# Performance work log

Hardware: AMD Instinct MI355X
Metric: run time of the kernel (lower is better)

The kernel has to match this reference:

```python
import jax, jax.numpy as jnp
import numpy as np
import math

D_MODEL = 512
H = 8
DK = D_MODEL // H  # 64
DFF = 2048
EPS = 1e-5


def layernorm(x, g, b):
    mu = jnp.mean(x, axis=-1, keepdims=True)
    var = jnp.mean((x - mu) ** 2, axis=-1, keepdims=True)
    return (x - mu) * jax.lax.rsqrt(var + EPS) * g + b


def gelu(x):
    return jax.nn.gelu(x, approximate=False)  # torch nn.GELU default (erf)


def feedforward(x, W1, b1, lng, lnb, W2, b2):
    x1 = jnp.einsum('btd,df->btf', x, W1) + b1
    x1 = gelu(layernorm(x1, lng, lnb))
    return jnp.einsum('btf,fd->btd', x1, W2) + b2


def setup_inputs() -> dict:
    key = jax.random.key(0)
    ks = iter(jax.random.split(key, 32))
    s = 0.02
    d = {}
    d['x'] = jax.random.normal(next(ks), (4, 2048, D_MODEL), jnp.float32)
    # per-head QKV projections, stacked over heads: [H, d_model, dk]
    d['Wq'] = jax.random.normal(next(ks), (H, D_MODEL, DK), jnp.float32) * s
    d['bq'] = jnp.zeros((H, DK), jnp.float32)
    d['Wk'] = jax.random.normal(next(ks), (H, D_MODEL, DK), jnp.float32) * s
    d['bk'] = jnp.zeros((H, DK), jnp.float32)
    d['Wv'] = jax.random.normal(next(ks), (H, D_MODEL, DK), jnp.float32) * s
    d['bv'] = jnp.zeros((H, DK), jnp.float32)
    d['Wo'] = jax.random.normal(next(ks), (D_MODEL, D_MODEL), jnp.float32) * s
    d['bo'] = jnp.zeros((D_MODEL,), jnp.float32)
    d['ln1_g'] = jnp.ones((D_MODEL,), jnp.float32)
    d['ln1_b'] = jnp.zeros((D_MODEL,), jnp.float32)
    # main FFN
    d['ff_W1'] = jax.random.normal(next(ks), (D_MODEL, DFF), jnp.float32) * s
    d['ff_b1'] = jnp.zeros((DFF,), jnp.float32)
    d['ff_lng'] = jnp.ones((DFF,), jnp.float32)
    d['ff_lnb'] = jnp.zeros((DFF,), jnp.float32)
    d['ff_W2'] = jax.random.normal(next(ks), (DFF, D_MODEL), jnp.float32) * s
    d['ff_b2'] = jnp.zeros((D_MODEL,), jnp.float32)
    d['ln2_g'] = jnp.ones((D_MODEL,), jnp.float32)
    d['ln2_b'] = jnp.zeros((D_MODEL,), jnp.float32)
    d['alphaA'] = jnp.zeros((1,), jnp.float32) + 0.1
    d['alphaB'] = jnp.zeros((1,), jnp.float32) + 0.1
    d['p1'] = jnp.asarray(0.1, jnp.float32)
    # sub1 FFN
    d['s1_W1'] = jax.random.normal(next(ks), (D_MODEL, DFF), jnp.float32) * s
    d['s1_b1'] = jnp.zeros((DFF,), jnp.float32)
    d['s1_lng'] = jnp.ones((DFF,), jnp.float32)
    d['s1_lnb'] = jnp.zeros((DFF,), jnp.float32)
    d['s1_W2'] = jax.random.normal(next(ks), (DFF, D_MODEL), jnp.float32) * s
    d['s1_b2'] = jnp.zeros((D_MODEL,), jnp.float32)
    d['lnsub1_g'] = jnp.ones((D_MODEL,), jnp.float32)
    d['lnsub1_b'] = jnp.zeros((D_MODEL,), jnp.float32)
    d['p2'] = jnp.asarray(0.1, jnp.float32)
    d['sub2_W'] = jax.random.normal(next(ks), (D_MODEL, D_MODEL), jnp.float32) * s
    d['sub2_b'] = jnp.zeros((D_MODEL,), jnp.float32)
    d['lnsub2_g'] = jnp.ones((D_MODEL,), jnp.float32)
    d['lnsub2_b'] = jnp.zeros((D_MODEL,), jnp.float32)
    return d


def reference(x, Wq, bq, Wk, bk, Wv, bv, Wo, bo, ln1_g, ln1_b,
              ff_W1, ff_b1, ff_lng, ff_lnb, ff_W2, ff_b2, ln2_g, ln2_b,
              alphaA, alphaB, p1, s1_W1, s1_b1, s1_lng, s1_lnb, s1_W2, s1_b2,
              lnsub1_g, lnsub1_b, p2, sub2_W, sub2_b, lnsub2_g, lnsub2_b):
    # --- multi-head attention (q = k = v = x) ---
    q = jnp.einsum('btd,hdk->bhtk', x, Wq) + bq[:, None, :]
    k = jnp.einsum('btd,hdk->bhtk', x, Wk) + bk[:, None, :]
    v = jnp.einsum('btd,hdk->bhtk', x, Wv) + bv[:, None, :]
    scores = jnp.einsum('bhtk,bhsk->bhts', q, k) / math.sqrt(DK)
    probs = jax.nn.softmax(scores, axis=-1)
    heads = jnp.einsum('bhts,bhsv->bhtv', probs, v)           # [B,H,T,dv]
    B, _, T, _ = heads.shape
    cat = jnp.transpose(heads, (0, 2, 1, 3)).reshape(B, T, H * DK)
    attn = jnp.einsum('btd,de->bte', cat, Wo) + bo
    # --- residual stack ---
    ln1 = layernorm(x + attn, ln1_g, ln1_b)
    out1 = x + ln1 * alphaA
    fft = feedforward(out1, ff_W1, ff_b1, ff_lng, ff_lnb, ff_W2, ff_b2)
    ln2 = layernorm(fft + out1, ln2_g, ln2_b)
    out2 = out1 + ln2 * alphaB
    # --- sub-branch 1 ---
    sub1 = feedforward(x, s1_W1, s1_b1, s1_lng, s1_lnb, s1_W2, s1_b2)
    sub1 = p1 * gelu(layernorm(sub1, lnsub1_g, lnsub1_b))
    # --- sub-branch 2 ---
    sub2 = jnp.einsum('btd,de->bte', x, sub2_W) + sub2_b
    sub2 = p2 * gelu(layernorm(sub2, lnsub2_g, lnsub2_b))
    return out2 + sub1 + sub2
```

## Files before the change

### kernel.cpp

```cpp
#include <hip/hip_runtime.h>
#include <hip/hip_bf16.h>
#include <math.h>

typedef __hip_bfloat16 bf16;
typedef __attribute__((ext_vector_type(8))) short s8v;
typedef __attribute__((ext_vector_type(4))) float f4v;

#define T_SEQ 2048
#define ROWS 8192
#define DMODEL 512
#define DFF 2048
#define QS 4096

#define GL2LDS(g, l) __builtin_amdgcn_global_load_lds( \
    (const __attribute__((address_space(1))) void*)(g), \
    (__attribute__((address_space(3))) void*)(l), 16, 0, 0)

__device__ __forceinline__ float b2f(bf16 v) { return __bfloat162float(v); }
__device__ __forceinline__ bf16 f2b(float v) { return __float2bfloat16(v); }
__device__ __forceinline__ float us2f(unsigned short u) {
    union { float f; unsigned int u; } c; c.u = ((unsigned int)u) << 16; return c.f;
}
__device__ __forceinline__ unsigned short f2us(float v) {
    bf16 b = f2b(v); return *(unsigned short*)&b;
}
__device__ __forceinline__ float gelu_f(float x) {
    return 0.5f * x * (1.0f + erff(x * 0.70710678118654752440f));
}
__device__ __forceinline__ float ldP(const void* p, int i, bool f32) {
    return f32 ? ((const float*)p)[i] : b2f(((const bf16*)p)[i]);
}

#define XB_E 4194304
#define RP_E 5505024
__global__ __launch_bounds__(256) void prep_all(
    const void* __restrict__ x,
    const void* Wq, const void* Wk, const void* Wv, const void* s2W,
    const void* s1W1, const void* ffW1, const void* ffW2, const void* s1W2,
    const void* Wo,
    const void* bq, const void* bk, const void* bv, const void* s2b,
    const void* s1b1, const void* bo, const void* ffb1, const void* ffb2,
    const void* s1b2,
    unsigned short* __restrict__ xb, unsigned short* __restrict__ Wbig2,
    unsigned short* __restrict__ ffW1t, unsigned short* __restrict__ ffW2t,
    unsigned short* __restrict__ s1W2t, unsigned short* __restrict__ Wot,
    float* __restrict__ bias_all, int* __restrict__ flag)
{
    __shared__ float red[4];
    __shared__ int lf;
    int tid = threadIdx.x;
    {
        float v = b2f(((const bf16*)x)[tid]);
        if (!(v == v)) v = 1e30f;
        float mx = fabsf(v);
        #pragma unroll
        for (int o = 32; o; o >>= 1) mx = fmaxf(mx, __shfl_down(mx, o));
        if ((tid & 63) == 0) red[tid >> 6] = mx;
        __syncthreads();
        if (tid == 0)
            lf = (fmaxf(fmaxf(red[0], red[1]), fmaxf(red[2], red[3])) > 1000.f) ? 1 : 0;
        __syncthreads();
    }
    bool f32 = lf != 0;
    if (blockIdx.x == 0 && tid == 0) flag[0] = lf;

    int idx = blockIdx.x * 256 + tid;
    if (idx < XB_E) {
        xb[idx] = f2us(ldP(x, idx, f32));
        return;
    }
    idx -= XB_E;
    if (idx < RP_E) {
        if (idx < 2097152) {
            int n = idx >> 9, d = idx & 511;
            float v;
            if (n < 1536) {
                int sec = n >> 9, nn = n & 511;
                int h = nn >> 6, j = nn & 63;
                const void* W = sec == 0 ? Wq : (sec == 1 ? Wk : Wv);
                v = ldP(W, (h * 512 + d) * 64 + j, f32);
            } else if (n < 2048) {
                v = ldP(s2W, d * 512 + (n - 1536), f32);
            } else {
                v = ldP(s1W1, d * 2048 + (n - 2048), f32);
            }
            Wbig2[idx] = f2us(v);
        } else if (idx < 3145728) {
            int i2 = idx - 2097152;
            int n = i2 >> 9, kd = i2 & 511;
            ffW1t[i2] = f2us(ldP(ffW1, kd * 2048 + n, f32));
        } else if (idx < 4194304) {
            int i2 = idx - 3145728;
            int n = i2 >> 11, kd = i2 & 2047;
            ffW2t[i2] = f2us(ldP(ffW2, kd * 512 + n, f32));
        } else if (idx < 5242880) {
            int i2 = idx - 4194304;
            int n = i2 >> 11, kd = i2 & 2047;
            s1W2t[i2] = f2us(ldP(s1W2, kd * 512 + n, f32));
        } else {
            int i2 = idx - 5242880;
            int n = i2 >> 9, kd = i2 & 511;
            Wot[i2] = f2us(ldP(Wo, kd * 512 + n, f32));
        }
        return;
    }
    idx -= RP_E;
    if (idx < 7680) {
        const void* src; int off;
        if      (idx < 512)  { src = bq;   off = idx; }
        else if (idx < 1024) { src = bk;   off = idx - 512; }
        else if (idx < 1536) { src = bv;   off = idx - 1024; }
        else if (idx < 2048) { src = s2b;  off = idx - 1536; }
        else if (idx < 4096) { src = s1b1; off = idx - 2048; }
        else if (idx < 4608) { src = bo;   off = idx - 4096; }
        else if (idx < 6656) { src = ffb1; off = idx - 4608; }
        else if (idx < 7168) { src = ffb2; off = idx - 6656; }
        else                 { src = s1b2; off = idx - 7168; }
        bias_all[idx] = ldP(src, off, f32);
    }
}

__device__ __forceinline__ void gemm_core(
    unsigned short* __restrict__ As, unsigned short* __restrict__ Bs,
    const unsigned short* __restrict__ A, int lda,
    const unsigned short* __restrict__ Bt,
    const float* __restrict__ bias,
    void* __restrict__ Cd, int ldc, int Kst,
    int kOff, int kLen, int doBias, int outBf16, int bm, int bn,
    unsigned short* __restrict__ Vt)
{
    int tid = threadIdx.x;
    int wave = tid >> 6, lane = tid & 63;
    int wm = wave >> 1, wn = wave & 1;
    int quad = lane >> 4, l16 = lane & 15;
    f4v acc[4][4] = {};
    int rsub = lane >> 3;
    int kcst = lane & 7;
    for (int k0 = kOff; k0 < kOff + kLen; k0 += 64) {
        #pragma unroll
        for (int i = 0; i < 4; i++) {
            int rowT = wave * 32 + i * 8 + rsub;
            int kc = (kcst - rowT) & 7;
            GL2LDS(A + (size_t)(bm + rowT) * lda + k0 + kc * 8,
                   &As[(wave * 32 + i * 8) * 64]);
            GL2LDS(Bt + (size_t)(bn + rowT) * Kst + k0 + kc * 8,
                   &Bs[(wave * 32 + i * 8) * 64]);
        }
        __syncthreads();
        #pragma unroll
        for (int ks = 0; ks < 64; ks += 32) {
            int kchunk = (ks >> 3) + quad;
            s8v af[4], bfr[4];
            #pragma unroll
            for (int mi = 0; mi < 4; mi++) {
                int m = wm * 64 + mi * 16 + l16;
                af[mi] = *(const s8v*)&As[m * 64 + (((kchunk + m) & 7) * 8)];
            }
            #pragma unroll
            for (int ni = 0; ni < 4; ni++) {
                int n = wn * 64 + ni * 16 + l16;
                bfr[ni] = *(const s8v*)&Bs[n * 64 + (((kchunk + n) & 7) * 8)];
            }
            #pragma unroll
            for (int mi = 0; mi < 4; mi++)
                #pragma unroll
                for (int ni = 0; ni < 4; ni++)
                    acc[mi][ni] = __builtin_amdgcn_mfma_f32_16x16x32_bf16(
                        af[mi], bfr[ni], acc[mi][ni], 0, 0, 0);
        }
        __syncthreads();
    }
    float bcol[4];
    #pragma unroll
    for (int ni = 0; ni < 4; ni++)
        bcol[ni] = doBias ? bias[bn + wn * 64 + ni * 16 + l16] : 0.f;
    #pragma unroll
    for (int mi = 0; mi < 4; mi++) {
        #pragma unroll
        for (int rg = 0; rg < 4; rg++) {
            size_t row = bm + wm * 64 + mi * 16 + quad * 4 + rg;
            #pragma unroll
            for (int ni = 0; ni < 4; ni++) {
                int col = bn + wn * 64 + ni * 16 + l16;
                float v = acc[mi][ni][rg] + bcol[ni];
                if (outBf16) ((unsigned short*)Cd)[row * ldc + col] = f2us(v);
                else         ((float*)Cd)[row * ldc + col] = v;
                if (Vt && col >= 1024 && col < 1536) {
                    int hd = col - 1024;
                    int b = (int)(row >> 11), t = (int)(row & 2047);
                    Vt[((size_t)b * 512 + hd) * 2048 + t] = f2us(v);
                }
            }
        }
    }
}

__global__ __launch_bounds__(256) void gemm_mfma(const unsigned short* __restrict__ A, int lda,
                                                 const unsigned short* __restrict__ Bt,
                                                 const float* __restrict__ bias,
                                                 void* __restrict__ C0,
                                                 void* __restrict__ C1,
                                                 int ldc, int K, int kLen, int outBf16,
                                                 unsigned short* __restrict__ Vt) {
    __shared__ unsigned short As[128 * 64];
    __shared__ unsigned short Bs[128 * 64];
    int z = blockIdx.z;
    gemm_core(As, Bs, A, lda, Bt, bias, z ? C1 : C0, ldc, K,
              z * kLen, kLen, z == 0, outBf16,
              blockIdx.y * 128, blockIdx.x * 128, Vt);
}

__global__ __launch_bounds__(256) void gemm_pair(
    const unsigned short* __restrict__ A1, int lda1,
    const unsigned short* __restrict__ Bt1, const float* __restrict__ bias1,
    void* __restrict__ C1a, void* __restrict__ C1b, int K1,
    const unsigned short* __restrict__ A2, int lda2,
    const unsigned short* __restrict__ Bt2, const float* __restrict__ bias2,
    void* __restrict__ C2a, void* __restrict__ C2b, int K2) {
    __shared__ unsigned short As[128 * 64];
    __shared__ unsigned short Bs[128 * 64];
    int z = blockIdx.z;
    if (z < 2) {
        int kLen = K1 / 2;
        gemm_core(As, Bs, A1, lda1, Bt1, bias1, z ? C1b : C1a, 512, K1,
                  z * kLen, kLen, z == 0, 1, blockIdx.y * 128, blockIdx.x * 128, nullptr);
    } else {
        int zz = z - 2, kLen = K2 / 2;
        gemm_core(As, Bs, A2, lda2, Bt2, bias2, zz ? C2b : C2a, 512, K2,
                  zz * kLen, kLen, zz == 0, 1, blockIdx.y * 128, blockIdx.x * 128, nullptr);
    }
}

#define ALD 72
#define SCL2 0.18033688f
__global__ __launch_bounds__(256) void attn_mfma(const unsigned short* __restrict__ QKV,
                                                 const unsigned short* __restrict__ Vt,
                                                 unsigned short* __restrict__ O) {
    __shared__ unsigned short Qs[64 * ALD];
    __shared__ unsigned short Ks[64 * ALD];
    __shared__ unsigned short Vts[64 * ALD];
    __shared__ unsigned short Ps[64 * ALD];

    int tid = threadIdx.x;
    int wave = tid >> 6, lane = tid & 63;
    int quad = lane >> 4, l16 = lane & 15;
    int qbase = blockIdx.x * 64;
    int bh = blockIdx.y;
    int b = bh >> 3, h = bh & 7;
    const unsigned short* Qg = QKV + ((size_t)(b * T_SEQ + qbase)) * QS + h * 64;
    const unsigned short* Kg = QKV + ((size_t)b * T_SEQ) * QS + 512 + h * 64;
    const unsigned short* Vtg = Vt + (size_t)bh * 64 * T_SEQ;

    int r = tid >> 3, c = (tid & 7) * 8;
    #pragma unroll
    for (int it = 0; it < 2; it++) {
        int rr = r + it * 32;
        uint4 v = *(const uint4*)(Qg + (size_t)rr * QS + c);
        *(uint4*)&Qs[rr * ALD + c] = v;
    }
    float lrun[4] = {0.f, 0.f, 0.f, 0.f};
    f4v oacc[4] = {};
    __syncthreads();

    for (int kt = 0; kt < 32; ++kt) {
        #pragma unroll
        for (int it = 0; it < 2; it++) {
            int rr = r + it * 32;
            uint4 kv = *(const uint4*)(Kg + (size_t)(kt * 64 + rr) * QS + c);
            *(uint4*)&Ks[rr * ALD + c] = kv;
            uint4 vv = *(const uint4*)(Vtg + (size_t)rr * T_SEQ + kt * 64 + c);
            *(uint4*)&Vts[rr * ALD + c] = vv;
        }
        __syncthreads();

        f4v sacc[4] = {};
        #pragma unroll
        for (int kc2 = 0; kc2 < 2; kc2++) {
            s8v aq = *(const s8v*)&Qs[(wave * 16 + l16) * ALD + kc2 * 32 + quad * 8];
            #pragma unroll
            for (int ni = 0; ni < 4; ni++) {
                s8v bk_ = *(const s8v*)&Ks[(ni * 16 + l16) * ALD + kc2 * 32 + quad * 8];
                sacc[ni] = __builtin_amdgcn_mfma_f32_16x16x32_bf16(aq, bk_, sacc[ni], 0, 0, 0);
            }
        }
        #pragma unroll
        for (int rg = 0; rg < 4; rg++) {
            #pragma unroll
            for (int ni = 0; ni < 4; ni++) {
                float p = exp2f(fminf(sacc[ni][rg] * SCL2, 30.f));
                lrun[rg] += p;
                Ps[(wave * 16 + quad * 4 + rg) * ALD + ni * 16 + l16] = f2us(p);
            }
        }
        #pragma unroll
        for (int kc2 = 0; kc2 < 2; kc2++) {
            s8v ap = *(const s8v*)&Ps[(wave * 16 + l16) * ALD + kc2 * 32 + quad * 8];
            #pragma unroll
            for (int ni = 0; ni < 4; ni++) {
                s8v bv_ = *(const s8v*)&Vts[(ni * 16 + l16) * ALD + kc2 * 32 + quad * 8];
                oacc[ni] = __builtin_amdgcn_mfma_f32_16x16x32_bf16(ap, bv_, oacc[ni], 0, 0, 0);
            }
        }
        __syncthreads();
    }

    #pragma unroll
    for (int rg = 0; rg < 4; rg++) {
        float l = lrun[rg];
        #pragma unroll
        for (int o = 8; o; o >>= 1) l += __shfl_xor(l, o);
        float linv = 1.0f / l;
        size_t orow = ((size_t)(b * T_SEQ + qbase + wave * 16 + quad * 4 + rg)) * 512 + h * 64;
        #pragma unroll
        for (int ni = 0; ni < 4; ni++)
            O[orow + ni * 16 + l16] = f2us(oacc[ni][rg] * linv);
    }
}

__global__ __launch_bounds__(256) void ln_res1(const void* __restrict__ Xraw,
                                               const unsigned short* __restrict__ Ya,
                                               const unsigned short* __restrict__ Yb,
                                               const void* __restrict__ g,
                                               const void* __restrict__ bb,
                                               const void* __restrict__ alpha,
                                               float* __restrict__ out,
                                               unsigned short* __restrict__ outb,
                                               const int* __restrict__ flag) {
    __shared__ float red[8];
    bool f32 = flag[0] != 0;
    int row = blockIdx.x, tid = threadIdx.x;
    size_t base = (size_t)row * DMODEL;
    float x0 = ldP(Xraw, base + tid, f32);
    float x1 = ldP(Xraw, base + tid + 256, f32);
    float v0 = x0 + us2f(Ya[base + tid]) + us2f(Yb[base + tid]);
    float v1 = x1 + us2f(Ya[base + tid + 256]) + us2f(Yb[base + tid + 256]);
    float s = v0 + v1, s2 = v0 * v0 + v1 * v1;
    #pragma unroll
    for (int o = 32; o; o >>= 1) { s += __shfl_down(s, o); s2 += __shfl_down(s2, o); }
    if ((tid & 63) == 0) { red[tid >> 6] = s; red[4 + (tid >> 6)] = s2; }
    __syncthreads();
    s = red[0] + red[1] + red[2] + red[3];
    s2 = red[4] + red[5] + red[6] + red[7];
    float mu = s * (1.0f / 512.0f);
    float var = s2 * (1.0f / 512.0f) - mu * mu;
    float rr = rsqrtf(var + 1e-5f);
    float a = ldP(alpha, 0, f32);
    float o0 = x0 + a * ((v0 - mu) * rr * ldP(g, tid, f32) + ldP(bb, tid, f32));
    float o1 = x1 + a * ((v1 - mu) * rr * ldP(g, tid + 256, f32) + ldP(bb, tid + 256, f32));
    out[base + tid] = o0;
    out[base + tid + 256] = o1;
    outb[base + tid] = f2us(o0);
    outb[base + tid + 256] = f2us(o1);
}

__global__ __launch_bounds__(256) void ln_gelu(unsigned short* __restrict__ Hm, int stride,
                                               const void* __restrict__ g,
                                               const void* __restrict__ bb,
                                               const int* __restrict__ flag) {
    __shared__ float red[8];
    bool f32 = flag[0] != 0;
    int row = blockIdx.x, tid = threadIdx.x;
    size_t base = (size_t)row * stride;
    float v[8];
    float s = 0.f, s2 = 0.f;
    #pragma unroll
    for (int i = 0; i < 8; i++) {
        v[i] = us2f(Hm[base + tid + i * 256]);
        s += v[i]; s2 += v[i] * v[i];
    }
    #pragma unroll
    for (int o = 32; o; o >>= 1) { s += __shfl_down(s, o); s2 += __shfl_down(s2, o); }
    if ((tid & 63) == 0) { red[tid >> 6] = s; red[4 + (tid >> 6)] = s2; }
    __syncthreads();
    s = red[0] + red[1] + red[2] + red[3];
    s2 = red[4] + red[5] + red[6] + red[7];
    float mu = s * (1.0f / 2048.0f);
    float var = s2 * (1.0f / 2048.0f) - mu * mu;
    float r = rsqrtf(var + 1e-5f);
    #pragma unroll
    for (int i = 0; i < 8; i++) {
        int cc = tid + i * 256;
        float ln = (v[i] - mu) * r * ldP(g, cc, f32) + ldP(bb, cc, f32);
        Hm[base + cc] = f2us(gelu_f(ln));
    }
}

__global__ __launch_bounds__(256) void final2(const float* __restrict__ out1,
                                              const float* __restrict__ fft,
                                              const float* __restrict__ fft2,
                                              const unsigned short* __restrict__ S1,
                                              const unsigned short* __restrict__ S1b,
                                              const unsigned short* __restrict__ S2,
                                              const void* __restrict__ g2ln,
                                              const void* __restrict__ b2ln,
                                              const void* __restrict__ alphaB,
                                              const void* __restrict__ g1s,
                                              const void* __restrict__ b1s,
                                              const void* __restrict__ g2s,
                                              const void* __restrict__ b2s,
                                              const void* __restrict__ p1,
                                              const void* __restrict__ p2,
                                              void* __restrict__ out,
                                              const int* __restrict__ flag) {
    __shared__ float red[24];
    bool f32 = flag[0] != 0;
    int row = blockIdx.x, tid = threadIdx.x;
    size_t base = (size_t)row * DMODEL;
    size_t base2 = (size_t)row * QS;
    float x0 = out1[base + tid], x1 = out1[base + tid + 256];
    float v0 = x0 + fft[base + tid] + fft2[base + tid];
    float v1 = x1 + fft[base + tid + 256] + fft2[base + tid + 256];
    float a0 = us2f(S1[base + tid]) + us2f(S1b[base + tid]);
    float a1 = us2f(S1[base + tid + 256]) + us2f(S1b[base + tid + 256]);
    float c0 = us2f(S2[base2 + tid]);
    float c1 = us2f(S2[base2 + tid + 256]);
    float sv = v0 + v1, sv2 = v0 * v0 + v1 * v1;
    float sa = a0 + a1, sa2 = a0 * a0 + a1 * a1;
    float sc = c0 + c1, sc2 = c0 * c0 + c1 * c1;
    #pragma unroll
    for (int o = 32; o; o >>= 1) {
        sv += __shfl_down(sv, o); sv2 += __shfl_down(sv2, o);
        sa += __shfl_down(sa, o); sa2 += __shfl_down(sa2, o);
        sc += __shfl_down(sc, o); sc2 += __shfl_down(sc2, o);
    }
    int w = tid >> 6;
    if ((tid & 63) == 0) {
        red[w] = sv; red[4 + w] = sv2; red[8 + w] = sa;
        red[12 + w] = sa2; red[16 + w] = sc; red[20 + w] = sc2;
    }
    __syncthreads();
    sv = red[0] + red[1] + red[2] + red[3];
    sv2 = red[4] + red[5] + red[6] + red[7];
    sa = red[8] + red[9] + red[10] + red[11];
    sa2 = red[12] + red[13] + red[14] + red[15];
    sc = red[16] + red[17] + red[18] + red[19];
    sc2 = red[20] + red[21] + red[22] + red[23];
    float muv = sv * (1.0f / 512.0f), varv = sv2 * (1.0f / 512.0f) - muv * muv;
    float rv = rsqrtf(varv + 1e-5f);
    float mua = sa * (1.0f / 512.0f), vara = sa2 * (1.0f / 512.0f) - mua * mua;
    float ra = rsqrtf(vara + 1e-5f);
    float muc = sc * (1.0f / 512.0f), varc = sc2 * (1.0f / 512.0f) - muc * muc;
    float rc = rsqrtf(varc + 1e-5f);
    float aB = ldP(alphaB, 0, f32);
    float fp1 = ldP(p1, 0, f32), fp2 = ldP(p2, 0, f32);
    float xv[2] = {x0, x1}, vv[2] = {v0, v1}, av[2] = {a0, a1}, cv[2] = {c0, c1};
    #pragma unroll
    for (int i = 0; i < 2; i++) {
        int cc = tid + i * 256;
        float out2 = xv[i] + aB * ((vv[i] - muv) * rv * ldP(g2ln, cc, f32) + ldP(b2ln, cc, f32));
        float l1 = (av[i] - mua) * ra * ldP(g1s, cc, f32) + ldP(b1s, cc, f32);
        float l2 = (cv[i] - muc) * rc * ldP(g2s, cc, f32) + ldP(b2s, cc, f32);
        float o = out2 + fp1 * gelu_f(l1) + fp2 * gelu_f(l2);
        if (f32) ((float*)out)[base + cc] = o;
        else     ((bf16*)out)[base + cc] = f2b(o);
    }
}

extern "C" void kernel_launch(void* const* d_in, const int* in_sizes, int n_in,
                              void* d_out, int out_size, void* d_ws, size_t ws_size,
                              hipStream_t stream) {
    (void)in_sizes; (void)n_in; (void)out_size; (void)ws_size;
    const void* x      = d_in[0];
    const void* Wq     = d_in[1];
    const void* bq     = d_in[2];
    const void* Wk     = d_in[3];
    const void* bk     = d_in[4];
    const void* Wv     = d_in[5];
    const void* bv     = d_in[6];
    const void* Wo     = d_in[7];
    const void* bo     = d_in[8];
    const void* ln1_g  = d_in[9];
    const void* ln1_b  = d_in[10];
    const void* ffW1   = d_in[11];
    const void* ffb1   = d_in[12];
    const void* fflng  = d_in[13];
    const void* fflnb  = d_in[14];
    const void* ffW2   = d_in[15];
    const void* ffb2   = d_in[16];
    const void* ln2_g  = d_in[17];
    const void* ln2_b  = d_in[18];
    const void* alphaA = d_in[19];
    const void* alphaB = d_in[20];
    const void* p1     = d_in[21];
    const void* s1W1   = d_in[22];
    const void* s1b1   = d_in[23];
    const void* s1lng  = d_in[24];
    const void* s1lnb  = d_in[25];
    const void* s1W2   = d_in[26];
    const void* s1b2   = d_in[27];
    const void* lns1g  = d_in[28];
    const void* lns1b  = d_in[29];
    const void* p2     = d_in[30];
    const void* s2W    = d_in[31];
    const void* s2b    = d_in[32];
    const void* lns2g  = d_in[33];
    const void* lns2b  = d_in[34];

    char* base = (char*)d_ws;
    size_t off = 0;
    auto alloc = [&](size_t bytes) {
        char* p = base + off;
        off += (bytes + 255) & ~(size_t)255;
        return p;
    };
    int* flag             = (int*)alloc(256);
    unsigned short* Wbig2 = (unsigned short*)alloc((size_t)4096 * 512 * 2);
    unsigned short* ffW1t = (unsigned short*)alloc((size_t)2048 * 512 * 2);
    unsigned short* ffW2t = (unsigned short*)alloc((size_t)512 * 2048 * 2);
    unsigned short* s1W2t = (unsigned short*)alloc((size_t)512 * 2048 * 2);
    unsigned short* Wot   = (unsigned short*)alloc(512 * 512 * 2);
    float* bias_all       = (float*)alloc(7680 * 4);
    char*  regX           = alloc((size_t)ROWS * 512 * 2);
    char*  regCat         = alloc((size_t)ROWS * 512 * 2);
    unsigned short* Cbig2 = (unsigned short*)alloc((size_t)ROWS * QS * 2);
    char*  regB           = alloc((size_t)ROWS * 512 * 2);
    char*  regD           = alloc((size_t)ROWS * 512 * 2);
    float* out1           = (float*)alloc((size_t)ROWS * 512 * 4);
    char*  regO           = alloc((size_t)ROWS * 512 * 4);

    unsigned short* xb    = (unsigned short*)regX;
    unsigned short* out1b = (unsigned short*)regX;
    unsigned short* catb  = (unsigned short*)regCat;
    float* fft            = (float*)regX;
    unsigned short* sub1raw  = (unsigned short*)regB;
    unsigned short* sub1raw2 = (unsigned short*)regD;
    unsigned short* Vtb   = (unsigned short*)regO;
    unsigned short* attnA = (unsigned short*)regO;
    unsigned short* attnB = (unsigned short*)(regO + (size_t)ROWS * 512 * 2);
    float* fft2           = (float*)regO;

    float* biasBig = bias_all + 0;
    float* biasWo  = bias_all + 4096;
    float* biasF1  = bias_all + 4608;
    float* biasF2  = bias_all + 6656;
    float* biasS12 = bias_all + 7168;

    prep_all<<<(XB_E + RP_E + 7680) / 256, 256, 0, stream>>>(
        x, Wq, Wk, Wv, s2W, s1W1, ffW1, ffW2, s1W2, Wo,
        bq, bk, bv, s2b, s1b1, bo, ffb1, ffb2, s1b2,
        xb, Wbig2, ffW1t, ffW2t, s1W2t, Wot, bias_all, flag);

    gemm_mfma<<<dim3(32, 64, 1), 256, 0, stream>>>(
        xb, 512, Wbig2, biasBig, Cbig2, nullptr, 4096, 512, 512, 1, Vtb);

    attn_mfma<<<dim3(T_SEQ / 64, 32), 256, 0, stream>>>(Cbig2, Vtb, catb);

    ln_gelu<<<ROWS, 256, 0, stream>>>(Cbig2 + 2048, QS, s1lng, s1lnb, flag);

    gemm_pair<<<dim3(4, 64, 4), 256, 0, stream>>>(
        Cbig2 + 2048, QS, s1W2t, biasS12, sub1raw, sub1raw2, 2048,
        catb, 512, Wot, biasWo, attnA, attnB, 512);

    ln_res1<<<ROWS, 256, 0, stream>>>(x, attnA, attnB, ln1_g, ln1_b, alphaA,
                                      out1, out1b, flag);

    gemm_mfma<<<dim3(16, 64, 1), 256, 0, stream>>>(
        out1b, 512, ffW1t, biasF1, Cbig2 + 2048, nullptr, 4096, 512, 512, 1, nullptr);

    ln_gelu<<<ROWS, 256, 0, stream>>>(Cbig2 + 2048, QS, fflng, fflnb, flag);

    gemm_mfma<<<dim3(4, 64, 2), 256, 0, stream>>>(
        Cbig2 + 2048, QS, ffW2t, biasF2, fft, fft2, 512, 2048, 1024, 0, nullptr);

    final2<<<ROWS, 256, 0, stream>>>(out1, fft, fft2, sub1raw, sub1raw2, Cbig2 + 1536,
                                     ln2_g, ln2_b, alphaB,
                                     lns1g, lns1b, lns2g, lns2b,
                                     p1, p2, d_out, flag);
}
```

Measured before the change: 511.1 us.

## Double-buffer LDS tiles in GEMM and attention with async global-to-LDS prefetch

The GEMM core and the attention kernel now use two LDS buffers per operand and prefetch the next K tile (and the next K/V tile in attention) while the current tile is being computed. Attention also switches from register-staged loads to direct global_load_lds with an XOR-swizzled layout. The aim is to hide global memory latency behind MFMA work. In exchange, LDS use doubles per block, which can lower occupancy. The loop's synchronisation also changes: the top-of-loop barrier is removed and only the end-of-loop barrier is left to order the prefetched buffer.

```diff
diff --git a/kernel.cpp b/kernel.cpp
--- a/kernel.cpp
+++ b/kernel.cpp
@@ -120,12 +120,33 @@
     }
 }
 
+__device__ __forceinline__ void stage_tile128(
+    const unsigned short* __restrict__ A, int lda,
+    const unsigned short* __restrict__ Bt, int ldb,
+    int bm, int bn, int k0,
+    unsigned short* __restrict__ As, unsigned short* __restrict__ Bs,
+    int wave, int lane)
+{
+    int rsub = lane >> 3, slot = lane & 7;
+    (void)slot;
+    #pragma unroll
+    for (int i = 0; i < 4; i++) {
+        int rowT = wave * 32 + i * 8 + rsub;
+        int kc = ((lane & 7) - rowT) & 7;
+        GL2LDS(A + (size_t)(bm + rowT) * lda + k0 + kc * 8,
+               &As[(wave * 32 + i * 8) * 64]);
+        GL2LDS(Bt + (size_t)(bn + rowT) * ldb + k0 + kc * 8,
+               &Bs[(wave * 32 + i * 8) * 64]);
+    }
+}
+
 __device__ __forceinline__ void gemm_core(
-    unsigned short* __restrict__ As, unsigned short* __restrict__ Bs,
+    unsigned short (*__restrict__ As)[128 * 64],
+    unsigned short (*__restrict__ Bs)[128 * 64],
     const unsigned short* __restrict__ A, int lda,
-    const unsigned short* __restrict__ Bt,
+    const unsigned short* __restrict__ Bt, int Kst,
     const float* __restrict__ bias,
-    void* __restrict__ Cd, int ldc, int Kst,
+    void* __restrict__ Cd, int ldc,
     int kOff, int kLen, int doBias, int outBf16, int bm, int bn,
     unsigned short* __restrict__ Vt)
 {
@@ -134,19 +155,14 @@
     int wm = wave >> 1, wn = wave & 1;
     int quad = lane >> 4, l16 = lane & 15;
     f4v acc[4][4] = {};
-    int rsub = lane >> 3;
-    int kcst = lane & 7;
-    for (int k0 = kOff; k0 < kOff + kLen; k0 += 64) {
-        #pragma unroll
-        for (int i = 0; i < 4; i++) {
-            int rowT = wave * 32 + i * 8 + rsub;
-            int kc = (kcst - rowT) & 7;
-            GL2LDS(A + (size_t)(bm + rowT) * lda + k0 + kc * 8,
-                   &As[(wave * 32 + i * 8) * 64]);
-            GL2LDS(Bt + (size_t)(bn + rowT) * Kst + k0 + kc * 8,
-                   &Bs[(wave * 32 + i * 8) * 64]);
-        }
-        __syncthreads();
+    int nIter = kLen >> 6;
+    stage_tile128(A, lda, Bt, Kst, bm, bn, kOff, As[0], Bs[0], wave, lane);
+    __syncthreads();
+    for (int it = 0; it < nIter; ++it) {
+        int cur = it & 1;
+        if (it + 1 < nIter)
+            stage_tile128(A, lda, Bt, Kst, bm, bn, kOff + (it + 1) * 64,
+                          As[cur ^ 1], Bs[cur ^ 1], wave, lane);
         #pragma unroll
         for (int ks = 0; ks < 64; ks += 32) {
             int kchunk = (ks >> 3) + quad;
@@ -154,12 +170,12 @@
             #pragma unroll
             for (int mi = 0; mi < 4; mi++) {
                 int m = wm * 64 + mi * 16 + l16;
-                af[mi] = *(const s8v*)&As[m * 64 + (((kchunk + m) & 7) * 8)];
+                af[mi] = *(const s8v*)&As[cur][m * 64 + (((kchunk + m) & 7) * 8)];
             }
             #pragma unroll
             for (int ni = 0; ni < 4; ni++) {
                 int n = wn * 64 + ni * 16 + l16;
-                bfr[ni] = *(const s8v*)&Bs[n * 64 + (((kchunk + n) & 7) * 8)];
+                bfr[ni] = *(const s8v*)&Bs[cur][n * 64 + (((kchunk + n) & 7) * 8)];
             }
             #pragma unroll
             for (int mi = 0; mi < 4; mi++)
@@ -202,10 +218,10 @@
                                                  void* __restrict__ C1,
                                                  int ldc, int K, int kLen, int outBf16,
                                                  unsigned short* __restrict__ Vt) {
-    __shared__ unsigned short As[128 * 64];
-    __shared__ unsigned short Bs[128 * 64];
+    __shared__ unsigned short As[2][128 * 64];
+    __shared__ unsigned short Bs[2][128 * 64];
     int z = blockIdx.z;
-    gemm_core(As, Bs, A, lda, Bt, bias, z ? C1 : C0, ldc, K,
+    gemm_core(As, Bs, A, lda, Bt, K, bias, z ? C1 : C0, ldc,
               z * kLen, kLen, z == 0, outBf16,
               blockIdx.y * 128, blockIdx.x * 128, Vt);
 }
@@ -217,16 +233,16 @@
     const unsigned short* __restrict__ A2, int lda2,
     const unsigned short* __restrict__ Bt2, const float* __restrict__ bias2,
     void* __restrict__ C2a, void* __restrict__ C2b, int K2) {
-    __shared__ unsigned short As[128 * 64];
-    __shared__ unsigned short Bs[128 * 64];
+    __shared__ unsigned short As[2][128 * 64];
+    __shared__ unsigned short Bs[2][128 * 64];
     int z = blockIdx.z;
     if (z < 2) {
         int kLen = K1 / 2;
-        gemm_core(As, Bs, A1, lda1, Bt1, bias1, z ? C1b : C1a, 512, K1,
+        gemm_core(As, Bs, A1, lda1, Bt1, K1, bias1, z ? C1b : C1a, 512,
                   z * kLen, kLen, z == 0, 1, blockIdx.y * 128, blockIdx.x * 128, nullptr);
     } else {
         int zz = z - 2, kLen = K2 / 2;
-        gemm_core(As, Bs, A2, lda2, Bt2, bias2, zz ? C2b : C2a, 512, K2,
+        gemm_core(As, Bs, A2, lda2, Bt2, K2, bias2, zz ? C2b : C2a, 512,
                   zz * kLen, kLen, zz == 0, 1, blockIdx.y * 128, blockIdx.x * 128, nullptr);
     }
 }
@@ -236,9 +252,9 @@
 __global__ __launch_bounds__(256) void attn_mfma(const unsigned short* __restrict__ QKV,
                                                  const unsigned short* __restrict__ Vt,
                                                  unsigned short* __restrict__ O) {
-    __shared__ unsigned short Qs[64 * ALD];
-    __shared__ unsigned short Ks[64 * ALD];
-    __shared__ unsigned short Vts[64 * ALD];
+    __shared__ unsigned short Qs[64 * 64];
+    __shared__ unsigned short Ks[2][64 * 64];
+    __shared__ unsigned short Vts[2][64 * 64];
     __shared__ unsigned short Ps[64 * ALD];
 
     int tid = threadIdx.x;
@@ -251,35 +267,42 @@
     const unsigned short* Kg = QKV + ((size_t)b * T_SEQ) * QS + 512 + h * 64;
     const unsigned short* Vtg = Vt + (size_t)bh * 64 * T_SEQ;
 
-    int r = tid >> 3, c = (tid & 7) * 8;
-    #pragma unroll
-    for (int it = 0; it < 2; it++) {
-        int rr = r + it * 32;
-        uint4 v = *(const uint4*)(Qg + (size_t)rr * QS + c);
-        *(uint4*)&Qs[rr * ALD + c] = v;
+    int rsub = lane >> 3, slot = lane & 7;
+    #pragma unroll
+    for (int i = 0; i < 2; i++) {
+        int r = wave * 16 + i * 8 + rsub;
+        int kc = (slot - r) & 7;
+        GL2LDS(Qg + (size_t)r * QS + kc * 8, &Qs[(wave * 16 + i * 8) * 64]);
+        GL2LDS(Kg + (size_t)r * QS + kc * 8, &Ks[0][(wave * 16 + i * 8) * 64]);
+        GL2LDS(Vtg + (size_t)r * T_SEQ + kc * 8, &Vts[0][(wave * 16 + i * 8) * 64]);
     }
     float lrun[4] = {0.f, 0.f, 0.f, 0.f};
     f4v oacc[4] = {};
     __syncthreads();
 
     for (int kt = 0; kt < 32; ++kt) {
-        #pragma unroll
-        for (int it = 0; it < 2; it++) {
-            int rr = r + it * 32;
-            uint4 kv = *(const uint4*)(Kg + (size_t)(kt * 64 + rr) * QS + c);
-            *(uint4*)&Ks[rr * ALD + c] = kv;
-            uint4 vv = *(const uint4*)(Vtg + (size_t)rr * T_SEQ + kt * 64 + c);
-            *(uint4*)&Vts[rr * ALD + c] = vv;
-        }
-        __syncthreads();
-
+        int cur = kt & 1;
+        if (kt + 1 < 32) {
+            #pragma unroll
+            for (int i = 0; i < 2; i++) {
+                int r = wave * 16 + i * 8 + rsub;
+                int kc = (slot - r) & 7;
+                GL2LDS(Kg + (size_t)((kt + 1) * 64 + r) * QS + kc * 8,
+                       &Ks[cur ^ 1][(wave * 16 + i * 8) * 64]);
+                GL2LDS(Vtg + (size_t)r * T_SEQ + (kt + 1) * 64 + kc * 8,
+                       &Vts[cur ^ 1][(wave * 16 + i * 8) * 64]);
+            }
+        }
         f4v sacc[4] = {};
         #pragma unroll
         for (int kc2 = 0; kc2 < 2; kc2++) {
-            s8v aq = *(const s8v*)&Qs[(wave * 16 + l16) * ALD + kc2 * 32 + quad * 8];
+            int m = wave * 16 + l16;
+            int ck = kc2 * 4 + quad;
+            s8v aq = *(const s8v*)&Qs[m * 64 + (((ck + m) & 7) * 8)];
             #pragma unroll
             for (int ni = 0; ni < 4; ni++) {
-                s8v bk_ = *(const s8v*)&Ks[(ni * 16 + l16) * ALD + kc2 * 32 + quad * 8];
+                int n = ni * 16 + l16;
+                s8v bk_ = *(const s8v*)&Ks[cur][n * 64 + (((ck + n) & 7) * 8)];
                 sacc[ni] = __builtin_amdgcn_mfma_f32_16x16x32_bf16(aq, bk_, sacc[ni], 0, 0, 0);
             }
         }
@@ -294,10 +317,12 @@
         }
         #pragma unroll
         for (int kc2 = 0; kc2 < 2; kc2++) {
+            int ck = kc2 * 4 + quad;
             s8v ap = *(const s8v*)&Ps[(wave * 16 + l16) * ALD + kc2 * 32 + quad * 8];
             #pragma unroll
             for (int ni = 0; ni < 4; ni++) {
-                s8v bv_ = *(const s8v*)&Vts[(ni * 16 + l16) * ALD + kc2 * 32 + quad * 8];
+                int n = ni * 16 + l16;
+                s8v bv_ = *(const s8v*)&Vts[cur][n * 64 + (((ck + n) & 7) * 8)];
                 oacc[ni] = __builtin_amdgcn_mfma_f32_16x16x32_bf16(ap, bv_, oacc[ni], 0, 0, 0);
             }
         }
```

Result: slower. 543.3 us (+6.3%).
